# Kernel optimization log

Hardware: AMD Instinct MI355X
Metric: run time of the kernel (lower is better)

Reference implementation:

```python
import jax, jax.numpy as jnp
import numpy as np

B, C, H, W = 64, 3, 512, 512
MAX_HOLES = 5
MAX_LEN = 170  # int(H * 1/3), exclusive upper bound for hole side length


def setup_inputs() -> dict:
    key = jax.random.key(0)
    k_img, k_n, k_y, k_x, k_h, k_w = jax.random.split(key, 6)
    return {
        "img": jax.random.normal(k_img, (B, C, H, W), dtype=jnp.float32),
        "num_holes": jax.random.randint(k_n, (B,), 0, MAX_HOLES, dtype=jnp.int32),
        "ys": jax.random.randint(k_y, (B, MAX_HOLES), 0, H, dtype=jnp.int32),
        "xs": jax.random.randint(k_x, (B, MAX_HOLES), 0, W, dtype=jnp.int32),
        "hs": jax.random.randint(k_h, (B, MAX_HOLES), 1, MAX_LEN, dtype=jnp.int32),
        "ws": jax.random.randint(k_w, (B, MAX_HOLES), 1, MAX_LEN, dtype=jnp.int32),
    }


def reference(img, num_holes, ys, xs, hs, ws):
    b, c, h, w = img.shape
    k = ys.shape[1]
    # Box edges, clamped to image bounds (matches torch clamp semantics).
    y1 = jnp.clip(ys - hs // 2, 0, h)[:, :, None]  # [B,K,1]
    y2 = jnp.clip(ys + hs // 2, 0, h)[:, :, None]
    x1 = jnp.clip(xs - ws // 2, 0, w)[:, :, None]
    x2 = jnp.clip(xs + ws // 2, 0, w)[:, :, None]
    rows = jnp.arange(h)[None, None, :]  # [1,1,H]
    cols = jnp.arange(w)[None, None, :]  # [1,1,W]
    in_y = (rows >= y1) & (rows < y2)  # [B,K,H]
    in_x = (cols >= x1) & (cols < x2)  # [B,K,W]
    # Only the first num_holes[i] boxes are active for sample i.
    active = (jnp.arange(k)[None, :] < num_holes[:, None])  # [B,K]
    inside = (in_y[:, :, :, None] & in_x[:, :, None, :]) & active[:, :, None, None]  # [B,K,H,W]
    mask = ~jnp.any(inside, axis=1)  # [B,H,W] True = keep pixel
    return img * mask[:, None, :, :].astype(img.dtype)
```

## Files before the change

kernel.cpp:

```cpp
#include <hip/hip_runtime.h>


#define BB 64
#define CC 3
#define HH 512
#define WW 512
#define KK 5
#define W4 (WW / 4)
#define W8 (WW / 8)
#define PLANE4 (HH * W4)

typedef float v4f __attribute__((ext_vector_type(4)));

__global__ __launch_bounds__(256) void cutout_kernel(
    const v4f* __restrict__ img,
    const int* __restrict__ num_holes,
    const int* __restrict__ ys,
    const int* __restrict__ xs,
    const int* __restrict__ hs,
    const int* __restrict__ ws,
    v4f* __restrict__ out)
{
    int idx = blockIdx.x * blockDim.x + threadIdx.x;

    int b   = idx >> 15;
    int rem = idx & 32767;
    int y   = rem >> 6;
    int x8  = rem & 63;
    int x0  = x8 << 3;

    int n = num_holes[b];

    float m[8];
#pragma unroll
    for (int j = 0; j < 8; ++j) m[j] = 1.0f;

    for (int k = 0; k < n; ++k) {
        int yc = ys[b * KK + k];
        int xc = xs[b * KK + k];
        int hh = hs[b * KK + k];
        int wv = ws[b * KK + k];
        int y1 = max(0, yc - hh / 2);
        int y2 = min(HH, yc + hh / 2);
        if (y >= y1 && y < y2) {
            int x1 = max(0, xc - wv / 2);
            int x2 = min(WW, xc + wv / 2);
#pragma unroll
            for (int j = 0; j < 8; ++j) {
                int xx = x0 + j;
                if (xx >= x1 && xx < x2) m[j] = 0.0f;
            }
        }
    }

    size_t p = (size_t)b * (CC * PLANE4) + (size_t)y * W4 + (size_t)(x8 << 1);
#pragma unroll
    for (int c = 0; c < CC; ++c) {
        size_t q = p + (size_t)c * PLANE4;
        v4f a = __builtin_nontemporal_load(&img[q]);
        v4f d = __builtin_nontemporal_load(&img[q + 1]);
        a.x *= m[0]; a.y *= m[1]; a.z *= m[2]; a.w *= m[3];
        d.x *= m[4]; d.y *= m[5]; d.z *= m[6]; d.w *= m[7];
        __builtin_nontemporal_store(a, &out[q]);
        __builtin_nontemporal_store(d, &out[q + 1]);
    }
}

extern "C" void kernel_launch(void* const* d_in, const int* in_sizes, int n_in,
                              void* d_out, int out_size, void* d_ws, size_t ws_size,
                              hipStream_t stream) {
    const v4f* img         = (const v4f*)d_in[0];
    const int* num_holes   = (const int*)d_in[1];
    const int* ys          = (const int*)d_in[2];
    const int* xs          = (const int*)d_in[3];
    const int* hs          = (const int*)d_in[4];
    const int* ws          = (const int*)d_in[5];
    v4f* out               = (v4f*)d_out;

    int total = BB * HH * W8;
    int block = 256;
    int grid  = total / block;
    cutout_kernel<<<grid, block, 0, stream>>>(img, num_holes, ys, xs, hs, ws, out);
}
```

Baseline: 83.60 us.

## Map one thread per float4 per channel plane with a 2D grid

Work is now split so each thread handles a single float4 in one channel plane, using a 2D grid indexed by (position, batch*channel), instead of 8 pixels across all 3 channels. Nontemporal loads and stores are replaced with plain loads and stores. This raises thread-level parallelism and keeps accesses fully coalesced, at the cost of recomputing the hole mask three times (once per channel) and launching three times as many threads.

```diff
diff --git a/kernel.cpp b/kernel.cpp
--- a/kernel.cpp
+++ b/kernel.cpp
@@ -7,7 +7,6 @@
 #define WW 512
 #define KK 5
 #define W4 (WW / 4)
-#define W8 (WW / 8)
 #define PLANE4 (HH * W4)
 
 typedef float v4f __attribute__((ext_vector_type(4)));
@@ -21,20 +20,15 @@
     const int* __restrict__ ws,
     v4f* __restrict__ out)
 {
-    int idx = blockIdx.x * blockDim.x + threadIdx.x;
+    int plane = blockIdx.y;
+    int b     = plane / 3;
+    int pos   = blockIdx.x * 256 + threadIdx.x;
+    int y     = pos >> 7;
+    int x0    = (pos & 127) << 2;
 
-    int b   = idx >> 15;
-    int rem = idx & 32767;
-    int y   = rem >> 6;
-    int x8  = rem & 63;
-    int x0  = x8 << 3;
+    float m0 = 1.0f, m1 = 1.0f, m2 = 1.0f, m3 = 1.0f;
 
     int n = num_holes[b];
-
-    float m[8];
-#pragma unroll
-    for (int j = 0; j < 8; ++j) m[j] = 1.0f;
-
     for (int k = 0; k < n; ++k) {
         int yc = ys[b * KK + k];
         int xc = xs[b * KK + k];
@@ -42,28 +36,21 @@
         int wv = ws[b * KK + k];
         int y1 = max(0, yc - hh / 2);
         int y2 = min(HH, yc + hh / 2);
-        if (y >= y1 && y < y2) {
-            int x1 = max(0, xc - wv / 2);
-            int x2 = min(WW, xc + wv / 2);
-#pragma unroll
-            for (int j = 0; j < 8; ++j) {
-                int xx = x0 + j;
-                if (xx >= x1 && xx < x2) m[j] = 0.0f;
-            }
+        int x1 = max(0, xc - wv / 2);
+        int x2 = min(WW, xc + wv / 2);
+        bool iny = (y >= y1) & (y < y2);
+        if (iny) {
+            if ((x0 + 0) >= x1 && (x0 + 0) < x2) m0 = 0.0f;
+            if ((x0 + 1) >= x1 && (x0 + 1) < x2) m1 = 0.0f;
+            if ((x0 + 2) >= x1 && (x0 + 2) < x2) m2 = 0.0f;
+            if ((x0 + 3) >= x1 && (x0 + 3) < x2) m3 = 0.0f;
         }
     }
 
-    size_t p = (size_t)b * (CC * PLANE4) + (size_t)y * W4 + (size_t)(x8 << 1);
-#pragma unroll
-    for (int c = 0; c < CC; ++c) {
-        size_t q = p + (size_t)c * PLANE4;
-        v4f a = __builtin_nontemporal_load(&img[q]);
-        v4f d = __builtin_nontemporal_load(&img[q + 1]);
-        a.x *= m[0]; a.y *= m[1]; a.z *= m[2]; a.w *= m[3];
-        d.x *= m[4]; d.y *= m[5]; d.z *= m[6]; d.w *= m[7];
-        __builtin_nontemporal_store(a, &out[q]);
-        __builtin_nontemporal_store(d, &out[q + 1]);
-    }
+    size_t q = (size_t)plane * PLANE4 + (size_t)pos;
+    v4f v = img[q];
+    v.x *= m0; v.y *= m1; v.z *= m2; v.w *= m3;
+    out[q] = v;
 }
 
 extern "C" void kernel_launch(void* const* d_in, const int* in_sizes, int n_in,
@@ -77,8 +64,6 @@
     const int* ws          = (const int*)d_in[5];
     v4f* out               = (v4f*)d_out;
 
-    int total = BB * HH * W8;
-    int block = 256;
-    int grid  = total / block;
-    cutout_kernel<<<grid, block, 0, stream>>>(img, num_holes, ys, xs, hs, ws, out);
+    dim3 grid(PLANE4 / 256, BB * CC);
+    cutout_kernel<<<grid, dim3(256), 0, stream>>>(img, num_holes, ys, xs, hs, ws, out);
 }
```

New measurement: 73.07 us. -12.6%, faster.
